# Optimization experiments

Measured on AMD Instinct MI355X. Metric: run time of the kernel, lower is better.

Reference implementation:

```python
import jax, jax.numpy as jnp
import numpy as np

N_ITEMS = 100000
N_USERS = 16384
HIST = 50
TEXT_DIM = 256
GCN_DIM = 128
HIDDEN_DIM = 512
TOWER_DIM = 128


def _l2norm(x, eps=1e-12):
    # F.normalize(dim=1): x / max(||x||, eps)
    n = jnp.sqrt(jnp.sum(x * x, axis=1, keepdims=True))
    return x / jnp.maximum(n, eps)


def setup_inputs() -> dict:
    key = jax.random.key(0)
    ks = jax.random.split(key, 10)
    s1i = 1.0 / np.sqrt(TEXT_DIM + GCN_DIM)
    s2i = 1.0 / np.sqrt(HIDDEN_DIM)
    s1u = 1.0 / np.sqrt(GCN_DIM + TOWER_DIM)
    return {
        "item_text_emb": jax.random.normal(ks[0], (N_ITEMS, TEXT_DIM), jnp.float32),
        "gcn_item_emb": jax.random.normal(ks[1], (N_ITEMS, GCN_DIM), jnp.float32),
        "gcn_user_emb": jax.random.normal(ks[2], (N_USERS, GCN_DIM), jnp.float32),
        "hist_idx": jax.random.randint(ks[3], (N_USERS, HIST), 0, N_ITEMS),
        "W1i": jax.random.normal(ks[4], (TEXT_DIM + GCN_DIM, HIDDEN_DIM), jnp.float32) * s1i,
        "b1i": jnp.zeros((HIDDEN_DIM,), jnp.float32),
        "W2i": jax.random.normal(ks[5], (HIDDEN_DIM, TOWER_DIM), jnp.float32) * s2i,
        "b2i": jnp.zeros((TOWER_DIM,), jnp.float32),
        "W1u": jax.random.normal(ks[6], (GCN_DIM + TOWER_DIM, HIDDEN_DIM), jnp.float32) * s1u,
        "b1u": jnp.zeros((HIDDEN_DIM,), jnp.float32),
        "W2u": jax.random.normal(ks[7], (HIDDEN_DIM, TOWER_DIM), jnp.float32) * s2i,
        "b2u": jnp.zeros((TOWER_DIM,), jnp.float32),
    }


def reference(item_text_emb, gcn_item_emb, gcn_user_emb, hist_idx,
              W1i, b1i, W2i, b2i, W1u, b1u, W2u, b2u):
    # encode_items: MLP over concat(text, gcn) features, then L2 normalize
    item_feat = jnp.concatenate([item_text_emb, gcn_item_emb], axis=1)  # [N_items, text+gcn]
    h = jax.nn.relu(item_feat @ W1i + b1i)
    item_emb = _l2norm(h @ W2i + b2i)  # [N_items, TOWER_DIM]
    # encode_users: per-user gather of history item embeddings + mean pooling
    hist = jnp.mean(item_emb[hist_idx], axis=1)  # [N_users, TOWER_DIM]
    fused = jnp.concatenate([gcn_user_emb, hist], axis=1)
    hu = jax.nn.relu(fused @ W1u + b1u)
    user_emb = _l2norm(hu @ W2u + b2u)  # [N_users, TOWER_DIM]
    return user_emb
```

## Files before the change

kernel.cpp:

```cpp
#include <hip/hip_runtime.h>
#include <hip/hip_bf16.h>

#define HIST 50
#define N_ITEMS 100000
#define N_USERS 16384

typedef __bf16 bf8 __attribute__((ext_vector_type(8)));
typedef float  f4  __attribute__((ext_vector_type(4)));
typedef float  f4v __attribute__((ext_vector_type(4)));

__device__ __forceinline__ unsigned short f2bf(float x) {
    unsigned u = __builtin_bit_cast(unsigned, x);
    u += 0x7fffu + ((u >> 16) & 1u);
    return (unsigned short)(u >> 16);
}
__device__ __forceinline__ float bf2f(unsigned b) {
    unsigned u = b << 16;
    return __builtin_bit_cast(float, u);
}

__global__ void pack_weights(const float* __restrict__ W1i, const float* __restrict__ W2i,
                             const float* __restrict__ W1u, const float* __restrict__ W2u,
                             unsigned short* __restrict__ dstbase)
{
    int i = blockIdx.x * 256 + threadIdx.x;
    const float* W; unsigned short* dst; int N, KS, loc;
    if (i < 24576)      { W = W1i; dst = dstbase;          N = 512; KS = 12; loc = i; }
    else if (i < 32768) { W = W2i; dst = dstbase + 196608; N = 128; KS = 16; loc = i - 24576; }
    else if (i < 49152) { W = W1u; dst = dstbase + 262144; N = 512; KS = 8;  loc = i - 32768; }
    else                { W = W2u; dst = dstbase + 393216; N = 128; KS = 16; loc = i - 49152; }
    int l = loc & 63, fi = loc >> 6;
    int ks = fi % KS, nt = fi / KS;
    int q = l >> 4, c = l & 15;
    const float* src = W + (size_t)(ks * 32 + q * 8) * N + nt * 16 + c;
    unsigned o[4];
    #pragma unroll
    for (int k = 0; k < 4; ++k) {
        unsigned lo = f2bf(src[(2 * k) * N]);
        unsigned hi = f2bf(src[(2 * k + 1) * N]);
        o[k] = lo | (hi << 16);
    }
    uint4 v; v.x = o[0]; v.y = o[1]; v.z = o[2]; v.w = o[3];
    ((uint4*)dst)[(size_t)(nt * KS + ks) * 64 + l] = v;
}

template<int NR, int KS1, int ASTR, bool OUT_BF16>
__device__ __forceinline__ void tower_core(
    unsigned short* U, const float* b1s, const float* b2s, float* sumsq,
    const bf8* __restrict__ w1f, const bf8* __restrict__ w2f,
    void* __restrict__ outp, int row0, int nval, int tid)
{
    const int HSTR = 520;
    const int l = tid & 63, w = tid >> 6;
    const int q = l >> 4, c = l & 15;

    f4 acc1[NR][4];
    #pragma unroll
    for (int i = 0; i < NR; ++i)
        #pragma unroll
        for (int j = 0; j < 4; ++j) acc1[i][j] = (f4)0.0f;

    const unsigned short* ap = U + c * ASTR + q * 8;
    bf8 bcur[4], bnxt[4];
    #pragma unroll
    for (int nt = 0; nt < 4; ++nt)
        bcur[nt] = w1f[(size_t)((w * 4 + nt) * KS1 + 0) * 64 + l];
    #pragma unroll
    for (int ks = 0; ks < KS1; ++ks) {
        if (ks + 1 < KS1) {
            #pragma unroll
            for (int nt = 0; nt < 4; ++nt)
                bnxt[nt] = w1f[(size_t)((w * 4 + nt) * KS1 + ks + 1) * 64 + l];
        }
        bf8 a[NR];
        #pragma unroll
        for (int rt = 0; rt < NR; ++rt)
            a[rt] = *(const bf8*)(ap + rt * 16 * ASTR + ks * 32);
        #pragma unroll
        for (int rt = 0; rt < NR; ++rt)
            #pragma unroll
            for (int nt = 0; nt < 4; ++nt)
                acc1[rt][nt] = __builtin_amdgcn_mfma_f32_16x16x32_bf16(a[rt], bcur[nt], acc1[rt][nt], 0, 0, 0);
        #pragma unroll
        for (int nt = 0; nt < 4; ++nt) bcur[nt] = bnxt[nt];
    }
    __syncthreads();

    #pragma unroll
    for (int nt = 0; nt < 4; ++nt) {
        int col = w * 64 + nt * 16 + c;
        float bias = b1s[col];
        #pragma unroll
        for (int rt = 0; rt < NR; ++rt)
            #pragma unroll
            for (int reg = 0; reg < 4; ++reg) {
                float h = fmaxf(acc1[rt][nt][reg] + bias, 0.0f);
                U[(rt * 16 + q * 4 + reg) * HSTR + col] = f2bf(h);
            }
    }
    __syncthreads();

    constexpr int NR2 = NR / 2;
    const int rg = w >> 2, jj = w & 3;
    f4 acc2[NR2][2];
    #pragma unroll
    for (int i = 0; i < NR2; ++i) { acc2[i][0] = (f4)0.0f; acc2[i][1] = (f4)0.0f; }

    const unsigned short* hp = U + (size_t)(rg * NR2 * 16 + c) * HSTR + q * 8;
    bf8 ccur[2], cnxt[2];
    ccur[0] = w2f[(size_t)((jj * 2 + 0) * 16 + 0) * 64 + l];
    ccur[1] = w2f[(size_t)((jj * 2 + 1) * 16 + 0) * 64 + l];
    #pragma unroll
    for (int ks = 0; ks < 16; ++ks) {
        if (ks + 1 < 16) {
            cnxt[0] = w2f[(size_t)((jj * 2 + 0) * 16 + ks + 1) * 64 + l];
            cnxt[1] = w2f[(size_t)((jj * 2 + 1) * 16 + ks + 1) * 64 + l];
        }
        bf8 a[NR2];
        #pragma unroll
        for (int i = 0; i < NR2; ++i)
            a[i] = *(const bf8*)(hp + i * 16 * HSTR + ks * 32);
        #pragma unroll
        for (int i = 0; i < NR2; ++i) {
            acc2[i][0] = __builtin_amdgcn_mfma_f32_16x16x32_bf16(a[i], ccur[0], acc2[i][0], 0, 0, 0);
            acc2[i][1] = __builtin_amdgcn_mfma_f32_16x16x32_bf16(a[i], ccur[1], acc2[i][1], 0, 0, 0);
        }
        ccur[0] = cnxt[0]; ccur[1] = cnxt[1];
    }

    float v[NR2][2][4];
    #pragma unroll
    for (int i = 0; i < NR2; ++i)
        #pragma unroll
        for (int j = 0; j < 2; ++j) {
            float bias = b2s[jj * 32 + j * 16 + c];
            #pragma unroll
            for (int reg = 0; reg < 4; ++reg)
                v[i][j][reg] = acc2[i][j][reg] + bias;
        }
    #pragma unroll
    for (int i = 0; i < NR2; ++i)
        #pragma unroll
        for (int reg = 0; reg < 4; ++reg) {
            float s = v[i][0][reg] * v[i][0][reg] + v[i][1][reg] * v[i][1][reg];
            s += __shfl_xor(s, 1); s += __shfl_xor(s, 2);
            s += __shfl_xor(s, 4); s += __shfl_xor(s, 8);
            if (c == 0) atomicAdd(&sumsq[rg * NR2 * 16 + i * 16 + q * 4 + reg], s);
        }
    __syncthreads();
    #pragma unroll
    for (int i = 0; i < NR2; ++i)
        #pragma unroll
        for (int reg = 0; reg < 4; ++reg) {
            int row = rg * NR2 * 16 + i * 16 + q * 4 + reg;
            if (row < nval) {
                float inv = 1.0f / fmaxf(sqrtf(sumsq[row]), 1e-12f);
                #pragma unroll
                for (int j = 0; j < 2; ++j) {
                    int col = jj * 32 + j * 16 + c;
                    float o = v[i][j][reg] * inv;
                    if (OUT_BF16)
                        __builtin_nontemporal_store(f2bf(o),
                            ((unsigned short*)outp) + (size_t)(row0 + row) * 128 + col);
                    else
                        __builtin_nontemporal_store(o,
                            ((float*)outp) + (size_t)(row0 + row) * 128 + col);
                }
            }
        }
}

#define ASI 392
#define ASU 264

__global__ __launch_bounds__(512, 4) void item_kernel(
    const float* __restrict__ text, const float* __restrict__ gcn,
    const bf8* __restrict__ w1f, const float* __restrict__ b1,
    const bf8* __restrict__ w2f, const float* __restrict__ b2,
    unsigned short* __restrict__ item_bf)
{
    __shared__ __align__(16) unsigned short U[64 * 520];
    __shared__ float b1s[512], b2s[128], sumsq[64];
    const int tid = threadIdx.x;
    const int row0 = blockIdx.x * 64;
    const int nval = min(64, N_ITEMS - row0);
    const f4v* t4 = (const f4v*)text;
    const f4v* g4 = (const f4v*)gcn;
    #pragma unroll
    for (int j = 0; j < 8; ++j) {
        int idx = tid + j * 512; int r = idx >> 6, c4 = idx & 63;
        f4v x = (r < nval) ? __builtin_nontemporal_load(t4 + (size_t)(row0 + r) * 64 + c4)
                           : (f4v)0.0f;
        ushort4 s; s.x = f2bf(x[0]); s.y = f2bf(x[1]); s.z = f2bf(x[2]); s.w = f2bf(x[3]);
        *(ushort4*)(U + r * ASI + c4 * 4) = s;
    }
    #pragma unroll
    for (int j = 0; j < 4; ++j) {
        int idx = tid + j * 512; int r = idx >> 5, c4 = idx & 31;
        f4v x = (r < nval) ? __builtin_nontemporal_load(g4 + (size_t)(row0 + r) * 32 + c4)
                           : (f4v)0.0f;
        ushort4 s; s.x = f2bf(x[0]); s.y = f2bf(x[1]); s.z = f2bf(x[2]); s.w = f2bf(x[3]);
        *(ushort4*)(U + r * ASI + 256 + c4 * 4) = s;
    }
    b1s[tid] = b1[tid];
    if (tid < 128) b2s[tid] = b2[tid];
    if (tid < 64)  sumsq[tid] = 0.0f;
    __syncthreads();
    tower_core<4, 12, ASI, true>(U, b1s, b2s, sumsq, w1f, w2f, item_bf, row0, nval, tid);
}

__global__ __launch_bounds__(512, 4) void user_kernel(
    const float* __restrict__ gcnu, const int* __restrict__ hist,
    const unsigned short* __restrict__ item_bf,
    const bf8* __restrict__ w1f, const float* __restrict__ b1,
    const bf8* __restrict__ w2f, const float* __restrict__ b2,
    float* __restrict__ outp)
{
    __shared__ __align__(16) unsigned short U[32 * 520];
    __shared__ float b1s[512], b2s[128], sumsq[32];
    const int tid = threadIdx.x;
    const int u0 = blockIdx.x * 32;
    int* hist_s = (int*)(U + 32 * ASU);
    const f4v* g4 = (const f4v*)gcnu;
    #pragma unroll
    for (int j = 0; j < 2; ++j) {
        int idx = tid + j * 512; int r = idx >> 5, c4 = idx & 31;
        f4v x = __builtin_nontemporal_load(g4 + (size_t)(u0 + r) * 32 + c4);
        ushort4 s; s.x = f2bf(x[0]); s.y = f2bf(x[1]); s.z = f2bf(x[2]); s.w = f2bf(x[3]);
        *(ushort4*)(U + r * ASU + c4 * 4) = s;
    }
    for (int k = tid; k < 32 * HIST; k += 512)
        hist_s[k] = __builtin_nontemporal_load(hist + (size_t)u0 * HIST + k);
    b1s[tid] = b1[tid];
    if (tid < 128) b2s[tid] = b2[tid];
    if (tid < 32)  sumsq[tid] = 0.0f;
    __syncthreads();
    {
        const int u = tid >> 4, g = tid & 15;
        float f[8];
        #pragma unroll
        for (int k = 0; k < 8; ++k) f[k] = 0.0f;
        const int* hrow = hist_s + u * HIST;
        #pragma unroll 10
        for (int t = 0; t < HIST; ++t) {
            int id = hrow[t];
            uint4 x = *(const uint4*)(item_bf + (size_t)id * 128 + g * 8);
            unsigned vs[4] = {x.x, x.y, x.z, x.w};
            #pragma unroll
            for (int k = 0; k < 4; ++k) {
                f[2 * k]     += bf2f(vs[k] & 0xffffu);
                f[2 * k + 1] += bf2f(vs[k] >> 16);
            }
        }
        unsigned o[4];
        #pragma unroll
        for (int k = 0; k < 4; ++k)
            o[k] = (unsigned)f2bf(f[2 * k] * 0.02f) | ((unsigned)f2bf(f[2 * k + 1] * 0.02f) << 16);
        uint4 s; s.x = o[0]; s.y = o[1]; s.z = o[2]; s.w = o[3];
        *(uint4*)(U + u * ASU + 128 + g * 8) = s;
    }
    __syncthreads();
    tower_core<2, 8, ASU, false>(U, b1s, b2s, sumsq, w1f, w2f, outp, u0, 32, tid);
}

extern "C" void kernel_launch(void* const* d_in, const int* in_sizes, int n_in,
                              void* d_out, int out_size, void* d_ws, size_t ws_size,
                              hipStream_t stream) {
    const float* text = (const float*)d_in[0];
    const float* gcni = (const float*)d_in[1];
    const float* gcnu = (const float*)d_in[2];
    const int*   hist = (const int*)d_in[3];
    const float* W1i  = (const float*)d_in[4];
    const float* b1i  = (const float*)d_in[5];
    const float* W2i  = (const float*)d_in[6];
    const float* b2i  = (const float*)d_in[7];
    const float* W1u  = (const float*)d_in[8];
    const float* b1u  = (const float*)d_in[9];
    const float* W2u  = (const float*)d_in[10];
    const float* b2u  = (const float*)d_in[11];
    float* out = (float*)d_out;

    unsigned short* itemb = (unsigned short*)d_ws;
    unsigned short* pw = itemb + 12800000;

    pack_weights<<<224, 256, 0, stream>>>(W1i, W2i, W1u, W2u, pw);
    item_kernel<<<(N_ITEMS + 63) / 64, 512, 0, stream>>>(
        text, gcni, (const bf8*)pw, b1i, (const bf8*)(pw + 196608), b2i, itemb);
    user_kernel<<<N_USERS / 32, 512, 0, stream>>>(
        gcnu, hist, itemb, (const bf8*)(pw + 262144), b1u, (const bf8*)(pw + 393216), b2u, out);
}
```

Before: 327.0 us.

## Shrink item tile to 32 rows, drop nontemporal hints, preload history ids

```diff
diff --git a/kernel.cpp b/kernel.cpp
--- a/kernel.cpp
+++ b/kernel.cpp
@@ -7,7 +7,6 @@
 
 typedef __bf16 bf8 __attribute__((ext_vector_type(8)));
 typedef float  f4  __attribute__((ext_vector_type(4)));
-typedef float  f4v __attribute__((ext_vector_type(4)));
 
 __device__ __forceinline__ unsigned short f2bf(float x) {
     unsigned u = __builtin_bit_cast(unsigned, x);
@@ -48,7 +47,7 @@
 __device__ __forceinline__ void tower_core(
     unsigned short* U, const float* b1s, const float* b2s, float* sumsq,
     const bf8* __restrict__ w1f, const bf8* __restrict__ w2f,
-    void* __restrict__ outp, int row0, int nval, int tid)
+    void* __restrict__ outp, int row0, int tid)
 {
     const int HSTR = 520;
     const int l = tid & 63, w = tid >> 6;
@@ -153,19 +152,15 @@
         #pragma unroll
         for (int reg = 0; reg < 4; ++reg) {
             int row = rg * NR2 * 16 + i * 16 + q * 4 + reg;
-            if (row < nval) {
-                float inv = 1.0f / fmaxf(sqrtf(sumsq[row]), 1e-12f);
-                #pragma unroll
-                for (int j = 0; j < 2; ++j) {
-                    int col = jj * 32 + j * 16 + c;
-                    float o = v[i][j][reg] * inv;
-                    if (OUT_BF16)
-                        __builtin_nontemporal_store(f2bf(o),
-                            ((unsigned short*)outp) + (size_t)(row0 + row) * 128 + col);
-                    else
-                        __builtin_nontemporal_store(o,
-                            ((float*)outp) + (size_t)(row0 + row) * 128 + col);
-                }
+            float inv = 1.0f / fmaxf(sqrtf(sumsq[row]), 1e-12f);
+            #pragma unroll
+            for (int j = 0; j < 2; ++j) {
+                int col = jj * 32 + j * 16 + c;
+                float o = v[i][j][reg] * inv;
+                if (OUT_BF16)
+                    ((unsigned short*)outp)[(size_t)(row0 + row) * 128 + col] = f2bf(o);
+                else
+                    ((float*)outp)[(size_t)(row0 + row) * 128 + col] = o;
             }
         }
 }
@@ -179,34 +174,31 @@
     const bf8* __restrict__ w2f, const float* __restrict__ b2,
     unsigned short* __restrict__ item_bf)
 {
-    __shared__ __align__(16) unsigned short U[64 * 520];
-    __shared__ float b1s[512], b2s[128], sumsq[64];
+    __shared__ __align__(16) unsigned short U[32 * 520];
+    __shared__ float b1s[512], b2s[128], sumsq[32];
     const int tid = threadIdx.x;
-    const int row0 = blockIdx.x * 64;
-    const int nval = min(64, N_ITEMS - row0);
-    const f4v* t4 = (const f4v*)text;
-    const f4v* g4 = (const f4v*)gcn;
-    #pragma unroll
-    for (int j = 0; j < 8; ++j) {
+    const int row0 = blockIdx.x * 32;
+    const float4* t4 = (const float4*)text;
+    const float4* g4 = (const float4*)gcn;
+    #pragma unroll
+    for (int j = 0; j < 4; ++j) {
         int idx = tid + j * 512; int r = idx >> 6, c4 = idx & 63;
-        f4v x = (r < nval) ? __builtin_nontemporal_load(t4 + (size_t)(row0 + r) * 64 + c4)
-                           : (f4v)0.0f;
-        ushort4 s; s.x = f2bf(x[0]); s.y = f2bf(x[1]); s.z = f2bf(x[2]); s.w = f2bf(x[3]);
+        float4 x = t4[(size_t)(row0 + r) * 64 + c4];
+        ushort4 s; s.x = f2bf(x.x); s.y = f2bf(x.y); s.z = f2bf(x.z); s.w = f2bf(x.w);
         *(ushort4*)(U + r * ASI + c4 * 4) = s;
     }
     #pragma unroll
-    for (int j = 0; j < 4; ++j) {
+    for (int j = 0; j < 2; ++j) {
         int idx = tid + j * 512; int r = idx >> 5, c4 = idx & 31;
-        f4v x = (r < nval) ? __builtin_nontemporal_load(g4 + (size_t)(row0 + r) * 32 + c4)
-                           : (f4v)0.0f;
-        ushort4 s; s.x = f2bf(x[0]); s.y = f2bf(x[1]); s.z = f2bf(x[2]); s.w = f2bf(x[3]);
+        float4 x = g4[(size_t)(row0 + r) * 32 + c4];
+        ushort4 s; s.x = f2bf(x.x); s.y = f2bf(x.y); s.z = f2bf(x.z); s.w = f2bf(x.w);
         *(ushort4*)(U + r * ASI + 256 + c4 * 4) = s;
     }
     b1s[tid] = b1[tid];
     if (tid < 128) b2s[tid] = b2[tid];
-    if (tid < 64)  sumsq[tid] = 0.0f;
-    __syncthreads();
-    tower_core<4, 12, ASI, true>(U, b1s, b2s, sumsq, w1f, w2f, item_bf, row0, nval, tid);
+    if (tid < 32)  sumsq[tid] = 0.0f;
+    __syncthreads();
+    tower_core<2, 12, ASI, true>(U, b1s, b2s, sumsq, w1f, w2f, item_bf, row0, tid);
 }
 
 __global__ __launch_bounds__(512, 4) void user_kernel(
@@ -221,30 +213,31 @@
     const int tid = threadIdx.x;
     const int u0 = blockIdx.x * 32;
     int* hist_s = (int*)(U + 32 * ASU);
-    const f4v* g4 = (const f4v*)gcnu;
+    const float4* g4 = (const float4*)gcnu;
     #pragma unroll
     for (int j = 0; j < 2; ++j) {
         int idx = tid + j * 512; int r = idx >> 5, c4 = idx & 31;
-        f4v x = __builtin_nontemporal_load(g4 + (size_t)(u0 + r) * 32 + c4);
-        ushort4 s; s.x = f2bf(x[0]); s.y = f2bf(x[1]); s.z = f2bf(x[2]); s.w = f2bf(x[3]);
+        float4 x = g4[(size_t)(u0 + r) * 32 + c4];
+        ushort4 s; s.x = f2bf(x.x); s.y = f2bf(x.y); s.z = f2bf(x.z); s.w = f2bf(x.w);
         *(ushort4*)(U + r * ASU + c4 * 4) = s;
     }
     for (int k = tid; k < 32 * HIST; k += 512)
-        hist_s[k] = __builtin_nontemporal_load(hist + (size_t)u0 * HIST + k);
+        hist_s[k] = hist[(size_t)u0 * HIST + k];
     b1s[tid] = b1[tid];
     if (tid < 128) b2s[tid] = b2[tid];
     if (tid < 32)  sumsq[tid] = 0.0f;
     __syncthreads();
     {
         const int u = tid >> 4, g = tid & 15;
+        int ids[HIST];
+        #pragma unroll
+        for (int t = 0; t < HIST; ++t) ids[t] = hist_s[u * HIST + t];
         float f[8];
         #pragma unroll
         for (int k = 0; k < 8; ++k) f[k] = 0.0f;
-        const int* hrow = hist_s + u * HIST;
-        #pragma unroll 10
+        #pragma unroll
         for (int t = 0; t < HIST; ++t) {
-            int id = hrow[t];
-            uint4 x = *(const uint4*)(item_bf + (size_t)id * 128 + g * 8);
+            uint4 x = *(const uint4*)(item_bf + (size_t)ids[t] * 128 + g * 8);
             unsigned vs[4] = {x.x, x.y, x.z, x.w};
             #pragma unroll
             for (int k = 0; k < 4; ++k) {
@@ -260,7 +253,7 @@
         *(uint4*)(U + u * ASU + 128 + g * 8) = s;
     }
     __syncthreads();
-    tower_core<2, 8, ASU, false>(U, b1s, b2s, sumsq, w1f, w2f, outp, u0, 32, tid);
+    tower_core<2, 8, ASU, false>(U, b1s, b2s, sumsq, w1f, w2f, outp, u0, tid);
 }
 
 extern "C" void kernel_launch(void* const* d_in, const int* in_sizes, int n_in,
@@ -284,7 +277,7 @@
     unsigned short* pw = itemb + 12800000;
 
     pack_weights<<<224, 256, 0, stream>>>(W1i, W2i, W1u, W2u, pw);
-    item_kernel<<<(N_ITEMS + 63) / 64, 512, 0, stream>>>(
+    item_kernel<<<N_ITEMS / 32, 512, 0, stream>>>(
         text, gcni, (const bf8*)pw, b1i, (const bf8*)(pw + 196608), b2i, itemb);
     user_kernel<<<N_USERS / 32, 512, 0, stream>>>(
         gcnu, hist, itemb, (const bf8*)(pw + 262144), b1u, (const bf8*)(pw + 393216), b2u, out);
```

After: 305.7 us. 1.07x faster.
